# Kernel optimization log

Measured on AMD Instinct MI355X. Metric: run time of the kernel, lower is better.

Reference implementation:

```python
import jax, jax.numpy as jnp
import numpy as np

OBS_DIM, GOAL_DIM, NUM_SKILLS, ACTION_DIM = 256, 64, 16, 32
HIDDEN = 128
BATCH = 65536


def setup_inputs() -> dict:
    key = jax.random.key(0)
    ks = jax.random.split(key, 10)
    s = lambda k, shape, fan_in: jax.random.normal(k, shape, jnp.float32) * (1.0 / np.sqrt(fan_in))
    return {
        "obs": jax.random.normal(ks[0], (BATCH, OBS_DIM), jnp.float32),
        "goals": jax.random.normal(ks[1], (BATCH, GOAL_DIM), jnp.float32),
        # gate (AlphaNet) params
        "Wa1": s(ks[2], (OBS_DIM + GOAL_DIM, HIDDEN), OBS_DIM + GOAL_DIM),
        "ba1": jnp.zeros((HIDDEN,), jnp.float32),
        "Wa2": s(ks[3], (HIDDEN, NUM_SKILLS), HIDDEN),
        "ba2": jnp.zeros((NUM_SKILLS,), jnp.float32),
        # stacked executor params: [S, in, out]
        "W1": s(ks[4], (NUM_SKILLS, OBS_DIM, HIDDEN), OBS_DIM),
        "b1": jnp.zeros((NUM_SKILLS, HIDDEN), jnp.float32),
        "W2": s(ks[5], (NUM_SKILLS, HIDDEN, ACTION_DIM), HIDDEN),
        "b2": jnp.zeros((NUM_SKILLS, ACTION_DIM), jnp.float32),
    }


def reference(obs, goals, Wa1, ba1, Wa2, ba2, W1, b1, W2, b2):
    # gate: softmax(Linear(ReLU(Linear(cat(obs, goals)))))
    concat_input = jnp.concatenate([obs, goals], axis=-1)  # [B, O+G]
    ha = jax.nn.relu(concat_input @ Wa1 + ba1)             # [B, H]
    alphas = jax.nn.softmax(ha @ Wa2 + ba2, axis=-1)       # [B, S]

    # all experts as one grouped GEMM over stacked weights
    h = jax.nn.relu(jnp.einsum("bo,soh->bsh", obs, W1) + b1[None])  # [B, S, H]
    skill_outputs = jnp.einsum("bsh,sha->bsa", h, W2) + b2[None]    # [B, S, A]

    # weighted sum over skills
    mixed_action = jnp.einsum("bsa,bs->ba", skill_outputs, alphas)  # [B, A]
    return mixed_action, alphas
```

## Files before the change

kernel.cpp:

```cpp
#include <hip/hip_runtime.h>


typedef __attribute__((ext_vector_type(8))) short    bf16x8;
typedef __attribute__((ext_vector_type(4))) float    f32x4;
typedef __attribute__((ext_vector_type(4))) _Float16 f16x4;
using half2v = decltype(__builtin_amdgcn_cvt_pkrtz(0.f, 0.f));

#define GATE_W1_OFF   0
#define GATE_W2_OFF   81920
#define GATE_BA1_OFF  86016
#define GATE_BA2_OFF  86528
#define GATE_BYTES    86592
#define S_W1_STRIDE   528
#define S_W2_OFF      67584
#define S_W2_STRIDE   272
#define S_B1_OFF      76288
#define S_B2_OFF      76800
#define S_IMG         76928
#define ALPHA_TBL     76928
#define LDS_BYTES     163520

__device__ __forceinline__ unsigned short f2bf(float f) {
  unsigned u = __builtin_bit_cast(unsigned, f);
  return (unsigned short)((u + 0x7FFFu + ((u >> 16) & 1u)) >> 16);
}

__device__ __forceinline__ bf16x8 pack_bf8(f32x4 a, f32x4 b) {
  int4 r;
  asm("v_cvt_pk_bf16_f32 %0, %1, %2" : "=v"(r.x) : "v"(a[0]), "v"(a[1]));
  asm("v_cvt_pk_bf16_f32 %0, %1, %2" : "=v"(r.y) : "v"(a[2]), "v"(a[3]));
  asm("v_cvt_pk_bf16_f32 %0, %1, %2" : "=v"(r.z) : "v"(b[0]), "v"(b[1]));
  asm("v_cvt_pk_bf16_f32 %0, %1, %2" : "=v"(r.w) : "v"(b[2]), "v"(b[3]));
  return __builtin_bit_cast(bf16x8, r);
}

#define RELU_SCALE_PACK(dst, v, av, z)                                   \
  {                                                                      \
    half2v lo_ = __builtin_amdgcn_cvt_pkrtz((v)[0], (v)[1]);             \
    half2v hi_ = __builtin_amdgcn_cvt_pkrtz((v)[2], (v)[3]);             \
    lo_ = __builtin_elementwise_max(lo_, z) * (av);                      \
    hi_ = __builtin_elementwise_max(hi_, z) * (av);                      \
    dst[0] = (_Float16)lo_[0]; dst[1] = (_Float16)lo_[1];                \
    dst[2] = (_Float16)hi_[0]; dst[3] = (_Float16)hi_[1];                \
  }
#define RELU_PACK(dst, v, z)                                             \
  {                                                                      \
    half2v lo_ = __builtin_amdgcn_cvt_pkrtz((v)[0], (v)[1]);             \
    half2v hi_ = __builtin_amdgcn_cvt_pkrtz((v)[2], (v)[3]);             \
    lo_ = __builtin_elementwise_max(lo_, z);                             \
    hi_ = __builtin_elementwise_max(hi_, z);                             \
    dst[0] = (_Float16)lo_[0]; dst[1] = (_Float16)lo_[1];                \
    dst[2] = (_Float16)hi_[0]; dst[3] = (_Float16)hi_[1];                \
  }

__global__ void prep_weights(const float* __restrict__ Wa1, const float* __restrict__ Wa2,
                             const float* __restrict__ ba1, const float* __restrict__ ba2,
                             const float* __restrict__ W1,  const float* __restrict__ W2,
                             const float* __restrict__ b1,  const float* __restrict__ b2,
                             unsigned char* __restrict__ ws) {
  int i = blockIdx.x * 256 + threadIdx.x;
  if (i < 524288) {
    int s = i >> 15, r = i & 32767, h = r >> 8, o = r & 255;
    float v = W1[(s * 256 + o) * 128 + h];
    *(unsigned short*)(ws + GATE_BYTES + s * S_IMG + h * S_W1_STRIDE + 2 * o) = f2bf(v);
  } else if (i < 589824) {
    int j = i - 524288, s = j >> 12, r = j & 4095, a = r >> 7, h = r & 127;
    float v = W2[(s * 128 + h) * 32 + a];
    *(_Float16*)(ws + GATE_BYTES + s * S_IMG + S_W2_OFF + a * S_W2_STRIDE + 2 * h) =
        (_Float16)v;
  } else if (i < 630784) {
    int j = i - 589824, h = j / 320, o = j - h * 320;
    float v = Wa1[o * 128 + h];
    *(unsigned short*)(ws + GATE_W1_OFF + h * 640 +
                       ((2 * o) ^ ((h & 7) << 4))) = f2bf(v);
  } else if (i < 632832) {
    int j = i - 630784, n = j >> 7, h = j & 127;
    float v = Wa2[h * 16 + n];
    *(_Float16*)(ws + GATE_W2_OFF + n * 256 +
                 ((2 * h) ^ ((n & 7) << 3))) = (_Float16)v;
  } else if (i < 634880) {
    int j = i - 632832, s = j >> 7, h = j & 127;
    *(float*)(ws + GATE_BYTES + s * S_IMG + S_B1_OFF + 4 * h) = b1[s * 128 + h];
  } else if (i < 635392) {
    int j = i - 634880, s = j >> 5, a = j & 31;
    *(float*)(ws + GATE_BYTES + s * S_IMG + S_B2_OFF + 4 * a) = b2[s * 32 + a];
  } else if (i < 635520) {
    int j = i - 635392;
    *(float*)(ws + GATE_BA1_OFF + 4 * j) = ba1[j];
  } else if (i < 635536) {
    int j = i - 635520;
    *(float*)(ws + GATE_BA2_OFF + 4 * j) = ba2[j];
  }
}

__device__ __forceinline__ void stage_lin(const unsigned char* gsrc, unsigned char* ldst,
                                          int tid, int bytes) {
  for (int off = tid * 16; off < bytes; off += 512 * 16) {
    __builtin_amdgcn_global_load_lds(
        (const __attribute__((address_space(1))) unsigned int*)(const void*)(gsrc + off),
        (__attribute__((address_space(3))) unsigned int*)(void*)(ldst + off), 16, 0, 0);
  }
}

__global__ __launch_bounds__(512, 1)
void mop_fused(const float* __restrict__ obs, const float* __restrict__ goals,
               const unsigned char* __restrict__ ws, float* __restrict__ dout) {
  extern __shared__ unsigned char smem[];
  const int tid  = threadIdx.x;
  const int lane = tid & 63;
  const int wave = tid >> 6;
  const int half = wave >> 2;
  const int pr   = wave & 3;
  const int l15  = lane & 15;
  const int g    = lane >> 4;
  const int swz4 = (lane & 7) << 4;
  const int swz3 = (lane & 7) << 3;
  const int htrot = (wave & 1) << 1;
  const int rowbase = blockIdx.x * 256 + pr * 64;

  float* out_mixed = dout;
  float* out_alpha = dout + 65536 * 32;

  const int lw1 = half * 33792 + l15 * S_W1_STRIDE + 16 * g;
  const int lw2 = S_W2_OFF + l15 * S_W2_STRIDE + 8 * g + half * 128;
  const int lb1 = S_B1_OFF + 256 * half + 16 * g;
  const int lb2 = S_B2_OFF + 16 * g;
  const int lrow = pr * 64 + l15;

  stage_lin(ws, smem, tid, GATE_BYTES);

  bf16x8 obsf[4][8];
  #pragma unroll
  for (int nb = 0; nb < 4; ++nb) {
    const float* rp = obs + (size_t)(rowbase + nb * 16 + l15) * 256 + 8 * g;
    #pragma unroll
    for (int t = 0; t < 8; ++t) {
      f32x4 a = *(const f32x4*)(rp + 32 * t);
      f32x4 c = *(const f32x4*)(rp + 32 * t + 4);
      obsf[nb][t] = pack_bf8(a, c);
    }
  }

  const half2v zh = __builtin_amdgcn_cvt_pkrtz(0.f, 0.f);
  f32x4 lacc[4];
  {
    bf16x8 goalf[4][2];
    #pragma unroll
    for (int nb = 0; nb < 4; ++nb) {
      const float* gp = goals + (size_t)(rowbase + nb * 16 + l15) * 64 + 8 * g;
      #pragma unroll
      for (int t = 0; t < 2; ++t) {
        f32x4 a = *(const f32x4*)(gp + 32 * t);
        f32x4 c = *(const f32x4*)(gp + 32 * t + 4);
        goalf[nb][t] = pack_bf8(a, c);
      }
    }

    __syncthreads();
    stage_lin(ws + GATE_BYTES, smem + GATE_BYTES, tid, S_IMG);

    #pragma unroll
    for (int p = 0; p < 2; ++p) {
      f32x4 gacc[2][4];
      #pragma unroll
      for (int ht = 0; ht < 4; ++ht) {
        f32x4 bias = *(const f32x4*)(smem + GATE_BA1_OFF + 256 * half + 64 * ht + 16 * g);
        gacc[0][ht] = bias; gacc[1][ht] = bias;
      }
      #pragma unroll
      for (int t = 0; t < 10; ++t) {
        bf16x8 bf0 = (t < 8) ? obsf[2 * p][t]     : goalf[2 * p][t - 8];
        bf16x8 bf1 = (t < 8) ? obsf[2 * p + 1][t] : goalf[2 * p + 1][t - 8];
        #pragma unroll
        for (int ht = 0; ht < 4; ++ht) {
          int row = 64 * half + 16 * ht + l15;
          bf16x8 af = *(const bf16x8*)(smem + GATE_W1_OFF + row * 640 +
                                       ((64 * t + 16 * g) ^ swz4));
          gacc[0][ht] = __builtin_amdgcn_mfma_f32_16x16x32_bf16(af, bf0, gacc[0][ht], 0, 0, 0);
          gacc[1][ht] = __builtin_amdgcn_mfma_f32_16x16x32_bf16(af, bf1, gacc[1][ht], 0, 0, 0);
        }
      }
      #pragma unroll
      for (int j = 0; j < 2; ++j) {
        const int nb = 2 * p + j;
        lacc[nb] = (half == 0) ? *(const f32x4*)(smem + GATE_BA2_OFF + 16 * g)
                               : f32x4{0.f, 0.f, 0.f, 0.f};
        #pragma unroll
        for (int ht = 0; ht < 4; ++ht) {
          f16x4 hf;
          RELU_PACK(hf, gacc[j][ht], zh);
          f16x4 wf = *(const f16x4*)(smem + GATE_W2_OFF + l15 * 256 +
                                     ((32 * (4 * half + ht) + 8 * g) ^ swz3));
          lacc[nb] = __builtin_amdgcn_mfma_f32_16x16x16f16(wf, hf, lacc[nb], 0, 0, 0);
        }
      }
    }
  }

  __syncthreads();
  #pragma unroll
  for (int nb = 0; nb < 4; ++nb)
    #pragma unroll
    for (int r = 0; r < 4; ++r)
      *(float*)(smem + wave * 4352 + nb * 1088 + (4 * g + r) * 68 + 4 * l15) = lacc[nb][r];
  __syncthreads();

  #pragma unroll
  for (int nb = 0; nb < 4; ++nb) {
    f32x4 l = lacc[nb];
    #pragma unroll
    for (int r = 0; r < 4; ++r)
      l[r] += *(const float*)(smem + (wave ^ 4) * 4352 + nb * 1088 + (4 * g + r) * 68 + 4 * l15);
    float m = fmaxf(fmaxf(l[0], l[1]), fmaxf(l[2], l[3]));
    m = fmaxf(m, __shfl_xor(m, 16, 64));
    m = fmaxf(m, __shfl_xor(m, 32, 64));
    f32x4 e;
    e[0] = __expf(l[0] - m); e[1] = __expf(l[1] - m);
    e[2] = __expf(l[2] - m); e[3] = __expf(l[3] - m);
    float ssum = e[0] + e[1] + e[2] + e[3];
    ssum += __shfl_xor(ssum, 16, 64);
    ssum += __shfl_xor(ssum, 32, 64);
    f32x4 al = e * (1.0f / ssum);
    if (half == 0) {
      *(f32x4*)(out_alpha + (size_t)(rowbase + nb * 16 + l15) * 16 + 4 * g) = al;
      #pragma unroll
      for (int r = 0; r < 4; ++r)
        *(_Float16*)(smem + ALPHA_TBL + (4 * g + r) * 544 + (lrow + nb * 16) * 2) =
            (_Float16)al[r];
    }
  }

  __syncthreads();

  f32x4 macc[4][2] = {};
  for (int s = 0; s < 16; ++s) {
    const unsigned char* buf = smem + ((s & 1) ? 0 : GATE_BYTES);
    if (s < 15) {
      unsigned char* nbuf = smem + (((s + 1) & 1) ? 0 : GATE_BYTES);
      stage_lin(ws + GATE_BYTES + (size_t)(s + 1) * S_IMG, nbuf, tid, S_IMG);
    }
    half2v ah[4];
    #pragma unroll
    for (int nb = 0; nb < 4; ++nb) {
      unsigned short raw = *(const unsigned short*)(
          smem + ALPHA_TBL + s * 544 + (lrow + nb * 16) * 2);
      __fp16 hv = __builtin_bit_cast(__fp16, raw);
      half2v a2; a2[0] = hv; a2[1] = hv;
      ah[nb] = a2;
    }

    const unsigned char* w1p = buf + lw1;
    const unsigned char* w2p = buf + lw2;

    __builtin_amdgcn_s_setprio(1);
    #pragma unroll
    for (int hti = 0; hti < 4; ++hti) {
      const int ht = (hti + htrot) & 3;
      f32x4 b1v = *(const f32x4*)(buf + lb1 + 64 * ht);
      f32x4 acc[4];
      #pragma unroll
      for (int nb = 0; nb < 4; ++nb) acc[nb] = b1v;
      const unsigned char* w1h = w1p + ht * 8448;
      #pragma unroll
      for (int t = 0; t < 8; ++t) {
        bf16x8 af = *(const bf16x8*)(w1h + t * 64);
        #pragma unroll
        for (int nb = 0; nb < 4; ++nb)
          acc[nb] = __builtin_amdgcn_mfma_f32_16x16x32_bf16(af, obsf[nb][t], acc[nb], 0, 0, 0);
      }
      f16x4 hf[4];
      #pragma unroll
      for (int nb = 0; nb < 4; ++nb) RELU_SCALE_PACK(hf[nb], acc[nb], ah[nb], zh);
      #pragma unroll
      for (int ta = 0; ta < 2; ++ta) {
        f16x4 wf = *(const f16x4*)(w2p + ta * 4352 + ht * 32);
        #pragma unroll
        for (int nb = 0; nb < 4; ++nb)
          macc[nb][ta] = __builtin_amdgcn_mfma_f32_16x16x16f16(wf, hf[nb], macc[nb][ta], 0, 0, 0);
      }
    }
    __builtin_amdgcn_s_setprio(0);
    if (half == 0) {
      #pragma unroll
      for (int ta = 0; ta < 2; ++ta) {
        f32x4 b2v = *(const f32x4*)(buf + lb2 + 64 * ta);
        #pragma unroll
        for (int nb = 0; nb < 4; ++nb) {
          float av = (float)ah[nb][0];
          macc[nb][ta] = macc[nb][ta] + b2v * av;
        }
      }
    }
    __syncthreads();
  }

  #pragma unroll
  for (int nb = 0; nb < 4; ++nb)
    #pragma unroll
    for (int ta = 0; ta < 2; ++ta)
      #pragma unroll
      for (int r = 0; r < 4; ++r)
        *(float*)(smem + wave * 8704 + nb * 2176 + (16 * ta + 4 * g + r) * 68 + 4 * l15) =
            macc[nb][ta][r];
  __syncthreads();
  #pragma unroll
  for (int j = 0; j < 2; ++j) {
    const int nb = 2 * half + j;
    #pragma unroll
    for (int ta = 0; ta < 2; ++ta) {
      f32x4 v = macc[nb][ta];
      #pragma unroll
      for (int r = 0; r < 4; ++r)
        v[r] += *(const float*)(smem + (wave ^ 4) * 8704 + nb * 2176 +
                                (16 * ta + 4 * g + r) * 68 + 4 * l15);
      *(f32x4*)(out_mixed + (size_t)(rowbase + nb * 16 + l15) * 32 + 16 * ta + 4 * g) = v;
    }
  }
}

extern "C" void kernel_launch(void* const* d_in, const int* in_sizes, int n_in,
                              void* d_out, int out_size, void* d_ws, size_t ws_size,
                              hipStream_t stream) {
  const float* obs   = (const float*)d_in[0];
  const float* goals = (const float*)d_in[1];
  const float* Wa1   = (const float*)d_in[2];
  const float* ba1   = (const float*)d_in[3];
  const float* Wa2   = (const float*)d_in[4];
  const float* ba2   = (const float*)d_in[5];
  const float* W1    = (const float*)d_in[6];
  const float* b1    = (const float*)d_in[7];
  const float* W2    = (const float*)d_in[8];
  const float* b2    = (const float*)d_in[9];
  unsigned char* ws  = (unsigned char*)d_ws;
  float* out = (float*)d_out;

  prep_weights<<<2483, 256, 0, stream>>>(Wa1, Wa2, ba1, ba2, W1, W2, b1, b2, ws);
  mop_fused<<<256, 512, LDS_BYTES, stream>>>(obs, goals, ws, out);
}
```

Baseline: 103.6 us.

## Raise launch-bound occupancy and process two hidden tiles per expert pass

Changes the launch bounds from one to two blocks per CU, which caps per-thread registers. The expert loop now computes two hidden tiles at once so more independent MFMA chains are in flight. Goal loads move inside the gate loop to shorten their live range, and the per-wave hidden-tile rotation is removed. The kernel still requests about 160 KB of LDS, so a second block likely cannot be co-resident. The tighter register cap also risks heavy spilling, since the bf16 obs fragments alone fill about 128 VGPRs.

Measured after the change: 99.51 us. 4.0% less time.

```diff
diff --git a/kernel.cpp b/kernel.cpp
--- a/kernel.cpp
+++ b/kernel.cpp
@@ -102,7 +102,7 @@
   }
 }
 
-__global__ __launch_bounds__(512, 1)
+__global__ __launch_bounds__(512, 2)
 void mop_fused(const float* __restrict__ obs, const float* __restrict__ goals,
                const unsigned char* __restrict__ ws, float* __restrict__ dout) {
   extern __shared__ unsigned char smem[];
@@ -115,7 +115,6 @@
   const int g    = lane >> 4;
   const int swz4 = (lane & 7) << 4;
   const int swz3 = (lane & 7) << 3;
-  const int htrot = (wave & 1) << 1;
   const int rowbase = blockIdx.x * 256 + pr * 64;
 
   float* out_mixed = dout;
@@ -143,56 +142,54 @@
 
   const half2v zh = __builtin_amdgcn_cvt_pkrtz(0.f, 0.f);
   f32x4 lacc[4];
-  {
-    bf16x8 goalf[4][2];
-    #pragma unroll
-    for (int nb = 0; nb < 4; ++nb) {
-      const float* gp = goals + (size_t)(rowbase + nb * 16 + l15) * 64 + 8 * g;
+
+  __syncthreads();
+  stage_lin(ws + GATE_BYTES, smem + GATE_BYTES, tid, S_IMG);
+
+  #pragma unroll
+  for (int p = 0; p < 2; ++p) {
+    bf16x8 goalf[2][2];
+    #pragma unroll
+    for (int j = 0; j < 2; ++j) {
+      const float* gp = goals + (size_t)(rowbase + (2 * p + j) * 16 + l15) * 64 + 8 * g;
       #pragma unroll
       for (int t = 0; t < 2; ++t) {
         f32x4 a = *(const f32x4*)(gp + 32 * t);
         f32x4 c = *(const f32x4*)(gp + 32 * t + 4);
-        goalf[nb][t] = pack_bf8(a, c);
-      }
-    }
-
-    __syncthreads();
-    stage_lin(ws + GATE_BYTES, smem + GATE_BYTES, tid, S_IMG);
-
-    #pragma unroll
-    for (int p = 0; p < 2; ++p) {
-      f32x4 gacc[2][4];
+        goalf[j][t] = pack_bf8(a, c);
+      }
+    }
+    f32x4 gacc[2][4];
+    #pragma unroll
+    for (int ht = 0; ht < 4; ++ht) {
+      f32x4 bias = *(const f32x4*)(smem + GATE_BA1_OFF + 256 * half + 64 * ht + 16 * g);
+      gacc[0][ht] = bias; gacc[1][ht] = bias;
+    }
+    #pragma unroll
+    for (int t = 0; t < 10; ++t) {
+      bf16x8 bf0 = (t < 8) ? obsf[2 * p][t]     : goalf[0][t - 8];
+      bf16x8 bf1 = (t < 8) ? obsf[2 * p + 1][t] : goalf[1][t - 8];
       #pragma unroll
       for (int ht = 0; ht < 4; ++ht) {
-        f32x4 bias = *(const f32x4*)(smem + GATE_BA1_OFF + 256 * half + 64 * ht + 16 * g);
-        gacc[0][ht] = bias; gacc[1][ht] = bias;
-      }
-      #pragma unroll
-      for (int t = 0; t < 10; ++t) {
-        bf16x8 bf0 = (t < 8) ? obsf[2 * p][t]     : goalf[2 * p][t - 8];
-        bf16x8 bf1 = (t < 8) ? obsf[2 * p + 1][t] : goalf[2 * p + 1][t - 8];
-        #pragma unroll
-        for (int ht = 0; ht < 4; ++ht) {
-          int row = 64 * half + 16 * ht + l15;
-          bf16x8 af = *(const bf16x8*)(smem + GATE_W1_OFF + row * 640 +
-                                       ((64 * t + 16 * g) ^ swz4));
-          gacc[0][ht] = __builtin_amdgcn_mfma_f32_16x16x32_bf16(af, bf0, gacc[0][ht], 0, 0, 0);
-          gacc[1][ht] = __builtin_amdgcn_mfma_f32_16x16x32_bf16(af, bf1, gacc[1][ht], 0, 0, 0);
-        }
-      }
-      #pragma unroll
-      for (int j = 0; j < 2; ++j) {
-        const int nb = 2 * p + j;
-        lacc[nb] = (half == 0) ? *(const f32x4*)(smem + GATE_BA2_OFF + 16 * g)
-                               : f32x4{0.f, 0.f, 0.f, 0.f};
-        #pragma unroll
-        for (int ht = 0; ht < 4; ++ht) {
-          f16x4 hf;
-          RELU_PACK(hf, gacc[j][ht], zh);
-          f16x4 wf = *(const f16x4*)(smem + GATE_W2_OFF + l15 * 256 +
-                                     ((32 * (4 * half + ht) + 8 * g) ^ swz3));
-          lacc[nb] = __builtin_amdgcn_mfma_f32_16x16x16f16(wf, hf, lacc[nb], 0, 0, 0);
-        }
+        int row = 64 * half + 16 * ht + l15;
+        bf16x8 af = *(const bf16x8*)(smem + GATE_W1_OFF + row * 640 +
+                                     ((64 * t + 16 * g) ^ swz4));
+        gacc[0][ht] = __builtin_amdgcn_mfma_f32_16x16x32_bf16(af, bf0, gacc[0][ht], 0, 0, 0);
+        gacc[1][ht] = __builtin_amdgcn_mfma_f32_16x16x32_bf16(af, bf1, gacc[1][ht], 0, 0, 0);
+      }
+    }
+    #pragma unroll
+    for (int j = 0; j < 2; ++j) {
+      const int nb = 2 * p + j;
+      lacc[nb] = (half == 0) ? *(const f32x4*)(smem + GATE_BA2_OFF + 16 * g)
+                             : f32x4{0.f, 0.f, 0.f, 0.f};
+      #pragma unroll
+      for (int ht = 0; ht < 4; ++ht) {
+        f16x4 hf;
+        RELU_PACK(hf, gacc[j][ht], zh);
+        f16x4 wf = *(const f16x4*)(smem + GATE_W2_OFF + l15 * 256 +
+                                   ((32 * (4 * half + ht) + 8 * g) ^ swz3));
+        lacc[nb] = __builtin_amdgcn_mfma_f32_16x16x16f16(wf, hf, lacc[nb], 0, 0, 0);
       }
     }
   }
@@ -240,6 +237,7 @@
       stage_lin(ws + GATE_BYTES + (size_t)(s + 1) * S_IMG, nbuf, tid, S_IMG);
     }
     half2v ah[4];
+    float av[4];
     #pragma unroll
     for (int nb = 0; nb < 4; ++nb) {
       unsigned short raw = *(const unsigned short*)(
@@ -247,6 +245,7 @@
       __fp16 hv = __builtin_bit_cast(__fp16, raw);
       half2v a2; a2[0] = hv; a2[1] = hv;
       ah[nb] = a2;
+      av[nb] = (float)hv;
     }
 
     const unsigned char* w1p = buf + lw1;
@@ -254,29 +253,37 @@
 
     __builtin_amdgcn_s_setprio(1);
     #pragma unroll
-    for (int hti = 0; hti < 4; ++hti) {
-      const int ht = (hti + htrot) & 3;
-      f32x4 b1v = *(const f32x4*)(buf + lb1 + 64 * ht);
-      f32x4 acc[4];
-      #pragma unroll
-      for (int nb = 0; nb < 4; ++nb) acc[nb] = b1v;
-      const unsigned char* w1h = w1p + ht * 8448;
+    for (int hp = 0; hp < 2; ++hp) {
+      f32x4 acc[4][2];
+      #pragma unroll
+      for (int hl = 0; hl < 2; ++hl) {
+        f32x4 b1v = *(const f32x4*)(buf + lb1 + (2 * hp + hl) * 64);
+        #pragma unroll
+        for (int nb = 0; nb < 4; ++nb) acc[nb][hl] = b1v;
+      }
       #pragma unroll
       for (int t = 0; t < 8; ++t) {
-        bf16x8 af = *(const bf16x8*)(w1h + t * 64);
-        #pragma unroll
-        for (int nb = 0; nb < 4; ++nb)
-          acc[nb] = __builtin_amdgcn_mfma_f32_16x16x32_bf16(af, obsf[nb][t], acc[nb], 0, 0, 0);
-      }
-      f16x4 hf[4];
-      #pragma unroll
-      for (int nb = 0; nb < 4; ++nb) RELU_SCALE_PACK(hf[nb], acc[nb], ah[nb], zh);
-      #pragma unroll
-      for (int ta = 0; ta < 2; ++ta) {
-        f16x4 wf = *(const f16x4*)(w2p + ta * 4352 + ht * 32);
-        #pragma unroll
-        for (int nb = 0; nb < 4; ++nb)
-          macc[nb][ta] = __builtin_amdgcn_mfma_f32_16x16x16f16(wf, hf[nb], macc[nb][ta], 0, 0, 0);
+        const unsigned char* w1t = w1p + t * 64;
+        #pragma unroll
+        for (int hl = 0; hl < 2; ++hl) {
+          bf16x8 af = *(const bf16x8*)(w1t + (2 * hp + hl) * 8448);
+          #pragma unroll
+          for (int nb = 0; nb < 4; ++nb)
+            acc[nb][hl] = __builtin_amdgcn_mfma_f32_16x16x32_bf16(af, obsf[nb][t], acc[nb][hl], 0, 0, 0);
+        }
+      }
+      #pragma unroll
+      for (int hl = 0; hl < 2; ++hl) {
+        f16x4 hf[4];
+        #pragma unroll
+        for (int nb = 0; nb < 4; ++nb) RELU_SCALE_PACK(hf[nb], acc[nb][hl], ah[nb], zh);
+        #pragma unroll
+        for (int ta = 0; ta < 2; ++ta) {
+          f16x4 wf = *(const f16x4*)(w2p + ta * 4352 + (2 * hp + hl) * 32);
+          #pragma unroll
+          for (int nb = 0; nb < 4; ++nb)
+            macc[nb][ta] = __builtin_amdgcn_mfma_f32_16x16x16f16(wf, hf[nb], macc[nb][ta], 0, 0, 0);
+        }
       }
     }
     __builtin_amdgcn_s_setprio(0);
@@ -285,10 +292,8 @@
       for (int ta = 0; ta < 2; ++ta) {
         f32x4 b2v = *(const f32x4*)(buf + lb2 + 64 * ta);
         #pragma unroll
-        for (int nb = 0; nb < 4; ++nb) {
-          float av = (float)ah[nb][0];
-          macc[nb][ta] = macc[nb][ta] + b2v * av;
-        }
+        for (int nb = 0; nb < 4; ++nb)
+          macc[nb][ta] = macc[nb][ta] + b2v * av[nb];
       }
     }
     __syncthreads();
```
